# Optimization experiments

Measured on AMD Instinct MI355X. Metric: run time of the kernel, lower is better.

## Reference

```python
import jax, jax.numpy as jnp
import numpy as np

L, B, P, D, H, DH, KV, M, S, A = 12, 8, 800, 1024, 8, 256, 1, 4096, 50, 32
ROPE_BASE = 10000.0
NEG = -1e30


def _rms(x, w):
    return (x * jax.lax.rsqrt(jnp.mean(x * x, -1, keepdims=True) + 1e-6)) * (1.0 + w)


def _rope(x, cos, sin):
    # x: [B,h,S,DH]; cos/sin: [B,1,S,DH//2]
    x1, x2 = jnp.split(x, 2, axis=-1)
    return jnp.concatenate([x1 * cos - x2 * sin, x2 * cos + x1 * sin], -1)


def setup_inputs() -> dict:
    key = jax.random.key(0)
    ks = iter(jax.random.split(key, 40))
    def nrm(shape, s=0.02):
        return jax.random.normal(next(ks), shape, jnp.float32) * s
    return {
        'prefix_pad_masks': jnp.ones((B, P), jnp.bool_),
        'x_t': jax.random.normal(next(ks), (B, S, A), jnp.float32),
        'timestep': jax.random.uniform(next(ks), (B,), jnp.float32),
        'dt': jnp.full((1,), 0.1, jnp.float32),
        'cache_k': nrm((L, B, KV, P, DH), 1.0),
        'cache_v': nrm((L, B, KV, P, DH), 1.0),
        'w_act_in': nrm((A, D)), 'b_act_in': jnp.zeros((D,), jnp.float32),
        'w_t1': nrm((D, D)), 'b_t1': jnp.zeros((D,), jnp.float32),
        'w_t2': nrm((D, D)), 'b_t2': jnp.zeros((D,), jnp.float32),
        'ln1_w': jnp.zeros((L, D), jnp.float32),
        'ada1_w': nrm((L, D, D)),
        'ln2_w': jnp.zeros((L, D), jnp.float32),
        'wq': nrm((L, D, H * DH)), 'wk': nrm((L, D, KV * DH)),
        'wv': nrm((L, D, KV * DH)), 'wo': nrm((L, H * DH, D)),
        'wg': nrm((L, D, M)), 'wu': nrm((L, D, M)), 'wd': nrm((L, M, D)),
        'lnf_w': jnp.zeros((D,), jnp.float32), 'adaf_w': nrm((D, D)),
        'w_act_out': nrm((D, A)), 'b_act_out': jnp.zeros((A,), jnp.float32),
    }


def reference(prefix_pad_masks, x_t, timestep, dt, cache_k, cache_v,
              w_act_in, b_act_in, w_t1, b_t1, w_t2, b_t2,
              ln1_w, ada1_w, ln2_w, wq, wk, wv, wo, wg, wu, wd,
              lnf_w, adaf_w, w_act_out, b_act_out):
    b, s, _ = x_t.shape
    p = prefix_pad_masks.shape[1]
    # --- embed_suffix: action projection + sinusoidal time -> MLP -> adaRMS cond ---
    suffix = x_t @ w_act_in + b_act_in                              # [B,S,D]
    half = D // 2
    freqs = jnp.exp(-jnp.log(jnp.float32(10000.0)) * jnp.arange(half, dtype=jnp.float32) / half)
    ang = timestep[:, None] * freqs[None, :]
    temb = jnp.concatenate([jnp.sin(ang), jnp.cos(ang)], -1)        # [B,D]
    cond = jax.nn.silu(temb @ w_t1 + b_t1) @ w_t2 + b_t2            # adarms_cond [B,D]
    # --- prefix-suffix 2D attention mask (make_att_2d_masks_trt) ---
    suffix_pad = jnp.ones((b, s), jnp.int32)
    suffix_att = jnp.concatenate([jnp.ones((b, 1), jnp.int32), jnp.zeros((b, s - 1), jnp.int32)], 1)
    cums = jnp.cumsum(suffix_att, 1)
    att2d = cums[:, None, :] <= cums[:, :, None]
    pad2d = (suffix_pad[:, None, :] * suffix_pad[:, :, None]).astype(bool)
    pre2d = jnp.broadcast_to(prefix_pad_masks[:, None, :], (b, s, p))
    full = jnp.concatenate([pre2d, att2d & pad2d], 2)               # [B,S,P+S]
    bias = jnp.where(full, 0.0, NEG)[:, None, :, :].astype(jnp.float32)
    # --- position ids: prefix offset + suffix cumsum - 1 ---
    offs = jnp.sum(prefix_pad_masks.astype(jnp.int32), -1)[:, None]
    pos = offs + jnp.cumsum(suffix_pad, 1) - 1                      # [B,S]
    inv = 1.0 / (ROPE_BASE ** (jnp.arange(0, DH, 2, dtype=jnp.float32) / DH))
    rang = pos[..., None].astype(jnp.float32) * inv                 # [B,S,DH/2]
    cos = jnp.cos(rang)[:, None]
    sin = jnp.sin(rang)[:, None]
    # --- gemma expert (eager attention over KV cache + suffix) ---
    h = suffix * jnp.sqrt(jnp.float32(D))
    def layer(hc, xs):
        l1, a1, l2, Wq, Wk, Wv, Wo, Wg, Wu, Wd, ck, cv = xs
        x = _rms(hc, l1) * (1.0 + (cond @ a1)[:, None, :])
        q = (x @ Wq).reshape(b, s, H, DH).transpose(0, 2, 1, 3)
        k = (x @ Wk).reshape(b, s, KV, DH).transpose(0, 2, 1, 3)
        v = (x @ Wv).reshape(b, s, KV, DH).transpose(0, 2, 1, 3)
        q = _rope(q, cos, sin)
        k = _rope(k, cos, sin)
        kf = jnp.repeat(jnp.concatenate([ck, k], 2), H // KV, 1)    # [B,H,P+S,DH]
        vf = jnp.repeat(jnp.concatenate([cv, v], 2), H // KV, 1)
        sc = jnp.einsum('bhsd,bhtd->bhst', q, kf) / jnp.sqrt(jnp.float32(DH)) + bias
        at = jax.nn.softmax(sc, -1)
        o = jnp.einsum('bhst,bhtd->bhsd', at, vf).transpose(0, 2, 1, 3).reshape(b, s, H * DH)
        hc = hc + o @ Wo
        x2 = _rms(hc, l2)
        hc = hc + (jax.nn.gelu(x2 @ Wg, approximate=True) * (x2 @ Wu)) @ Wd
        return hc, None
    h, _ = jax.lax.scan(layer, h, (ln1_w, ada1_w, ln2_w, wq, wk, wv, wo, wg, wu, wd, cache_k, cache_v))
    hf = _rms(h, lnf_w) * (1.0 + (cond @ adaf_w)[:, None, :])
    v_t = hf[:, -S:].astype(jnp.float32) @ w_act_out + b_act_out    # action_out_proj
    return x_t + dt.reshape(1, 1, 1) * v_t                          # Euler step
```

## Files before the change

kernel.cpp:

```cpp
#include <hip/hip_runtime.h>
#include <hip/hip_bf16.h>
#include <math.h>

#define NLAYER 12
#define NB 8
#define NP 800
#define ND 1024
#define NH 8
#define NDH 256
#define NM 4096
#define NS 50
#define NA 32
#define NKEYS 850
#define KPAD 896
#define NCH 7

typedef unsigned short ushort_t;
typedef unsigned int u32;
using f32x4  = __attribute__((ext_vector_type(4))) float;
using short8 = __attribute__((ext_vector_type(8))) short;

__device__ __forceinline__ u32 pack_bf2(float lo, float hi) {
  u32 a = __float_as_uint(lo);
  u32 b = __float_as_uint(hi);
  a += 0x7fffu + ((a >> 16) & 1u);
  b += 0x7fffu + ((b >> 16) & 1u);
  return (a >> 16) | (b & 0xffff0000u);
}
__device__ __forceinline__ ushort_t bf1(float x) {
  u32 a = __float_as_uint(x);
  a += 0x7fffu + ((a >> 16) & 1u);
  return (ushort_t)(a >> 16);
}
__device__ __forceinline__ float ubf(ushort_t h) {
  return __uint_as_float(((u32)h) << 16);
}
__device__ __forceinline__ void async_cp16(const void* g, const void* l) {
  __builtin_amdgcn_global_load_lds(
      (const __attribute__((address_space(1))) u32*)g,
      (__attribute__((address_space(3))) u32*)l, 16, 0, 0);
}
#define SWZ(row, c) ((c) ^ (((row) & 7) << 3))


__global__ void cvt_permute_kernel(const float* __restrict__ src, ushort_t* __restrict__ dst, long nrows) {
  long idx = (long)blockIdx.x * 256 + threadIdx.x;
  long row = idx >> 5;
  int t = (int)(idx & 31);
  if (row >= nrows) return;
  const float* s = src + row * 256 + t * 4;
  float4 lo = *reinterpret_cast<const float4*>(s);
  float4 hi = *reinterpret_cast<const float4*>(s + 128);
  ushort_t* d = dst + row * 256 + t * 8;
  *reinterpret_cast<uint4*>(d) =
      make_uint4(pack_bf2(lo.x, hi.x), pack_bf2(lo.y, hi.y),
                 pack_bf2(lo.z, hi.z), pack_bf2(lo.w, hi.w));
}

template<int MODE>
__global__ __launch_bounds__(256) void transpose_cvt(
    const float* __restrict__ src, long sz, ushort_t* __restrict__ dst, long dz,
    int R, int C, int ldd, int halfOff) {
  __shared__ float Ls[64][65];
  const float* s = src + (long)blockIdx.z * sz;
  ushort_t* d    = dst + (long)blockIdx.z * dz;
  int c0 = blockIdx.x * 64, r0 = blockIdx.y * 64;
  int t = threadIdx.x;
  int rr = t >> 4;
  int cc = (t & 15) * 4;
#pragma unroll
  for (int j = 0; j < 4; ++j) {
    int rl = rr + j * 16;
    int r = r0 + rl;
    float4 v = make_float4(0.f, 0.f, 0.f, 0.f);
    if (r < R) v = *reinterpret_cast<const float4*>(s + (long)r * C + c0 + cc);
    Ls[rl][cc] = v.x; Ls[rl][cc+1] = v.y; Ls[rl][cc+2] = v.z; Ls[rl][cc+3] = v.w;
  }
  __syncthreads();
  int dr = t >> 2;
  int rc = (t & 3) * 16;
  int cg = c0 + dr;
  long orow;
  if (MODE == 0)      orow = cg;
  else if (MODE == 1) orow = ((long)(cg >> 5) << 6) + (cg & 31) + halfOff;
  else                orow = (long)(cg & ~255) + ((cg & 127) << 1) + ((cg >> 7) & 1);
  ushort_t* drow = d + orow * ldd + r0 + rc;
#pragma unroll
  for (int i = 0; i < 16; i += 2) {
    int sr = r0 + rc + i;
    if (sr < R) {
      u32 p = pack_bf2(Ls[rc + i][dr], Ls[rc + i + 1][dr]);
      *reinterpret_cast<u32*>(drow + i) = p;
    }
  }
}


__global__ void temb_kernel(const float* __restrict__ ts, float* __restrict__ temb) {
  int idx = blockIdx.x * 256 + threadIdx.x;
  if (idx >= NB * ND) return;
  int b = idx >> 10, d = idx & 1023;
  int i = d & 511;
  float f = __expf(-logf(10000.f) * (float)i / 512.f);
  float ang = ts[b] * f;
  temb[idx] = (d < 512) ? sinf(ang) : cosf(ang);
}

__global__ void suffix_kernel(const float* __restrict__ x_t, const float* __restrict__ w,
                              const float* __restrict__ bias, float* __restrict__ h) {
  int m = blockIdx.x;
  __shared__ float xs[NA];
  if (threadIdx.x < NA) xs[threadIdx.x] = x_t[m * NA + threadIdx.x];
  __syncthreads();
  for (int n = threadIdx.x; n < ND; n += 256) {
    float acc = bias[n];
#pragma unroll
    for (int k = 0; k < NA; ++k) acc += xs[k] * w[k * ND + n];
    h[m * ND + n] = acc * 32.0f;
  }
}

__global__ void rope_table_kernel(float* __restrict__ cosT, float* __restrict__ sinT) {
  int idx = blockIdx.x * 256 + threadIdx.x;
  if (idx >= NS * 128) return;
  int s = idx >> 7, i = idx & 127;
  float inv = __expf(-(float)(2 * i) / 256.f * logf(10000.f));
  float ang = (float)(NP + s) * inv;
  cosT[idx] = cosf(ang);
  sinT[idx] = sinf(ang);
}

template<bool BFOUT>
__global__ void rms_kernel(float* __restrict__ hin, const float* __restrict__ slabs,
                           const float* __restrict__ w,
                           const float* __restrict__ ada, void* __restrict__ outv) {
  int m = blockIdx.x;
  int b = m / NS;
  int d0 = threadIdx.x * 4;
  float4 v = *reinterpret_cast<const float4*>(hin + (long)m * ND + d0);
  if (slabs) {
#pragma unroll
    for (int c = 0; c < 8; ++c) {
      float4 sv = *reinterpret_cast<const float4*>(slabs + ((long)c * 400 + m) * ND + d0);
      v.x += sv.x; v.y += sv.y; v.z += sv.z; v.w += sv.w;
    }
    *reinterpret_cast<float4*>(hin + (long)m * ND + d0) = v;
  }
  float ss = v.x*v.x + v.y*v.y + v.z*v.z + v.w*v.w;
#pragma unroll
  for (int off = 32; off > 0; off >>= 1) ss += __shfl_down(ss, off);
  __shared__ float red[4];
  int lane = threadIdx.x & 63, wid = threadIdx.x >> 6;
  if (lane == 0) red[wid] = ss;
  __syncthreads();
  float tot = red[0] + red[1] + red[2] + red[3];
  float r = rsqrtf(tot * (1.f / ND) + 1e-6f);
  float4 wv = *reinterpret_cast<const float4*>(w + d0);
  float4 o;
  o.x = v.x * r * (1.f + wv.x);
  o.y = v.y * r * (1.f + wv.y);
  o.z = v.z * r * (1.f + wv.z);
  o.w = v.w * r * (1.f + wv.w);
  if (ada) {
    float4 av = *reinterpret_cast<const float4*>(ada + (long)b * ND + d0);
    o.x *= (1.f + av.x); o.y *= (1.f + av.y); o.z *= (1.f + av.z); o.w *= (1.f + av.w);
  }
  if (BFOUT) {
    *reinterpret_cast<uint2*>((ushort_t*)outv + (long)m * ND + d0) =
        make_uint2(pack_bf2(o.x, o.y), pack_bf2(o.z, o.w));
  } else {
    *reinterpret_cast<float4*>((float*)outv + (long)m * ND + d0) = o;
  }
}

__global__ void final_fused(const float* __restrict__ hin, const float* __restrict__ slabs,
                            const float* __restrict__ lnf,
                            const float* __restrict__ adaf, const float* __restrict__ w,
                            const float* __restrict__ bias, const float* __restrict__ x_t,
                            const float* __restrict__ dt, float* __restrict__ out) {
  int m = blockIdx.x;
  int b = m / NS;
  int d0 = threadIdx.x * 4;
  __shared__ float hfs[ND];
  __shared__ float red[256];
  float4 v = *reinterpret_cast<const float4*>(hin + (long)m * ND + d0);
#pragma unroll
  for (int c = 0; c < 8; ++c) {
    float4 sv = *reinterpret_cast<const float4*>(slabs + ((long)c * 400 + m) * ND + d0);
    v.x += sv.x; v.y += sv.y; v.z += sv.z; v.w += sv.w;
  }
  float ss = v.x*v.x + v.y*v.y + v.z*v.z + v.w*v.w;
#pragma unroll
  for (int off = 32; off > 0; off >>= 1) ss += __shfl_down(ss, off);
  __shared__ float red4[4];
  int lane = threadIdx.x & 63, wid = threadIdx.x >> 6;
  if (lane == 0) red4[wid] = ss;
  __syncthreads();
  float tot = red4[0] + red4[1] + red4[2] + red4[3];
  float r = rsqrtf(tot * (1.f / ND) + 1e-6f);
  float4 wv = *reinterpret_cast<const float4*>(lnf + d0);
  float4 av = *reinterpret_cast<const float4*>(adaf + (long)b * ND + d0);
  hfs[d0]     = v.x * r * (1.f + wv.x) * (1.f + av.x);
  hfs[d0 + 1] = v.y * r * (1.f + wv.y) * (1.f + av.y);
  hfs[d0 + 2] = v.z * r * (1.f + wv.z) * (1.f + av.z);
  hfs[d0 + 3] = v.w * r * (1.f + wv.w) * (1.f + av.w);
  __syncthreads();
  int a = threadIdx.x & 31;
  int kg = threadIdx.x >> 5;
  float acc = 0.f;
  for (int k = kg; k < ND; k += 8) acc += hfs[k] * w[k * NA + a];
  red[threadIdx.x] = acc;
  __syncthreads();
// ... 131 lines not shown
  const int ci1 = 256 + ci0;
  const int row1 = ci1 >> 3;
  const int kc1 = (((ci1 & 7) ^ (row1 & 7)) << 3);
  int gra0 = m0 + row0; if (gra0 > M - 1) gra0 = M - 1;
  int gra1 = m0 + row1; if (gra1 > M - 1) gra1 = M - 1;
  const int n_0 = n0 + row0;
  const int n_1 = n0 + row1;

  auto stage = [&](int buf, int k0) {
    async_cp16(A + (long)gra0 * lda + k0 + kc0, (const char*)As[buf] + ci0 * 16);
    async_cp16(B + (long)n_0 * ldb + k0 + kc0, (const char*)Bs[buf] + ci0 * 16);
    async_cp16(A + (long)gra1 * lda + k0 + kc1, (const char*)As[buf] + ci1 * 16);
    async_cp16(B + (long)n_1 * ldb + k0 + kc1, (const char*)Bs[buf] + ci1 * 16);
  };

  stage(0, 0);
  __syncthreads();
  int cur = 0;
  for (int t = 0; t < 16; ++t) {
    if (t + 1 < 16) stage(cur ^ 1, (t + 1) * 64);
    const ushort_t* Ac = As[cur];
    const ushort_t* Bc = Bs[cur];
#pragma unroll
    for (int ks = 0; ks < 2; ++ks) {
      short8 af[2], bf[2];
#pragma unroll
      for (int mi = 0; mi < 2; ++mi) {
        int row = wm + mi * 16 + l15;
        af[mi] = *reinterpret_cast<const short8*>(&Ac[row * 64 + SWZ(row, ks * 32 + l4 * 8)]);
      }
#pragma unroll
      for (int ni = 0; ni < 2; ++ni) {
        int row = wn + ni * 16 + l15;
        bf[ni] = *reinterpret_cast<const short8*>(&Bc[row * 64 + SWZ(row, ks * 32 + l4 * 8)]);
      }
#pragma unroll
      for (int mi = 0; mi < 2; ++mi)
#pragma unroll
        for (int ni = 0; ni < 2; ++ni)
          acc[mi][ni] = __builtin_amdgcn_mfma_f32_16x16x32_bf16(af[mi], bf[ni], acc[mi][ni], 0, 0, 0);
    }
    __syncthreads();
    cur ^= 1;
  }

#pragma unroll
  for (int mi = 0; mi < 2; ++mi) {
#pragma unroll
    for (int ni = 0; ni < 2; ++ni) {
      int col = n0 + wn + ni * 16 + l15;
      int rb  = m0 + wm + mi * 16 + l4 * 4;
      float pv[4];
#pragma unroll
      for (int r = 0; r < 4; ++r) pv[r] = __shfl_xor(acc[mi][ni][r], 1);
#pragma unroll
      for (int r = 0; r < 4; ++r) {
        int row = rb + r;
        if (row >= 400) continue;
        int b = row / NS, s = row - b * NS;
        float v = acc[mi][ni][r];
        if (col < 2304) {
          int j = col & 255;
          int i = j >> 1;
          float c = cosT[s * 128 + i], sn = sinT[s * 128 + i];
          float o = (col & 1) ? (v * c + pv[r] * sn) : (v * c - pv[r] * sn);
          if (col < 2048)
            qTo[((long)((b << 3) + (col >> 8)) * NS + s) * 256 + j] = bf1(o);
          else
            k_new[(long)row * 256 + j] = bf1(o);
        } else {
          vT_l[((long)(b * 256 + (col - 2304))) * KPAD + NP + s] = bf1(v);
        }
      }
    }
  }
}

__global__ __launch_bounds__(256) void flash3_kernel(
    const ushort_t* __restrict__ qT,
    const ushort_t* __restrict__ kcache_l,
    const ushort_t* __restrict__ k_new,
    const ushort_t* __restrict__ vT_l,
    const ushort_t* __restrict__ zpad,
    ushort_t* __restrict__ opart, float* __restrict__ mpart, float* __restrict__ lpart) {
  const int flat = blockIdx.x + 64 * blockIdx.y;
  const int wgid = (flat & 7) * 56 + (flat >> 3);
  const int bh = wgid & 63;
  const int ch = wgid >> 6;
  const int b  = bh >> 3;
  const int tid = threadIdx.x;
  const int lane = tid & 63;
  const int w = tid >> 6;
  const int wm = (w >> 1) * 32;
  const int wnK = (w & 1) * 64;
  const int wnV = (w & 1) * 64;
  const int l15 = lane & 15;
  const int l4  = lane >> 4;

  __shared__ __align__(16) char lds[51200];
  ushort_t* KV0 = (ushort_t*)lds;
  ushort_t* KV1 = (ushort_t*)(lds + 16384);
  ushort_t* Ps  = (ushort_t*)(lds + 32768);
  float* SMm = (float*)(lds + 50176);
  float* SMl = (float*)(lds + 50688);

  short8 qf[4][2][2];
  {
    const ushort_t* qbase = qT + (long)bh * NS * 256;
#pragma unroll
    for (int mi = 0; mi < 2; ++mi) {
      int row = wm + mi * 16 + l15;
      int qr = row < NS ? row : NS - 1;
      const ushort_t* qrow = qbase + (long)qr * 256;
#pragma unroll
      for (int s = 0; s < 4; ++s)
#pragma unroll
        for (int ks = 0; ks < 2; ++ks)
          qf[s][mi][ks] = *reinterpret_cast<const short8*>(qrow + s * 64 + ks * 32 + l4 * 8);
    }
  }

  auto stageK = [&](ushort_t* buf, int s) {
#pragma unroll
    for (int i = 0; i < 4; ++i) {
      int ci = i * 256 + tid;
      int key = ch * 128 + (ci >> 3);
      int seg = (ci ^ (ci >> 3)) & 7;
      const ushort_t* src;
      if (key < NP)         src = kcache_l + ((long)(b * NP + key)) * 256 + s * 64 + seg * 8;
      else if (key < NKEYS) src = k_new + ((long)(b * NS + key - NP)) * 256 + s * 64 + seg * 8;
      else                  src = zpad + seg * 8;
      async_cp16(src, (char*)buf + ci * 16);
    }
  };
  auto stageV = [&](ushort_t* buf, int p) {
    int dh = p >> 1, ks2 = p & 1;
#pragma unroll
    for (int i = 0; i < 4; ++i) {
      int ci = i * 256 + tid;
      int dout = dh * 128 + (ci >> 3);
      int seg = (ci ^ (ci >> 3)) & 7;
      async_cp16(vT_l + ((long)(b * 256 + dout)) * KPAD + ch * 128 + ks2 * 64 + seg * 8,
                 (char*)buf + ci * 16);
    }
  };

  f32x4 s2[2][4] = {};
  stageK(KV0, 0);
  __syncthreads();
#pragma unroll
  for (int s = 0; s < 4; ++s) {
    ushort_t* buf = (s & 1) ? KV1 : KV0;
    ushort_t* nxt = (s & 1) ? KV0 : KV1;
    if (s < 3) stageK(nxt, s + 1);
    __builtin_amdgcn_s_setprio(1);
#pragma unroll
    for (int ks = 0; ks < 2; ++ks) {
      short8 bf[4];
#pragma unroll
      for (int ni = 0; ni < 4; ++ni) {
        int row = wnK + ni * 16 + l15;
        bf[ni] = *reinterpret_cast<const short8*>(&buf[row * 64 + SWZ(row, ks * 32 + l4 * 8)]);
      }
#pragma unroll
      for (int mi = 0; mi < 2; ++mi)
#pragma unroll
        for (int ni = 0; ni < 4; ++ni)
// ... 51 lines not shown
#pragma unroll
  for (int mi = 0; mi < 2; ++mi)
#pragma unroll
    for (int ni = 0; ni < 4; ++ni) {
      int colp = wnK + ni * 16 + l15;
#pragma unroll
      for (int r = 0; r < 4; ++r) {
        float e = __expf(s2[mi][ni][r] - mrow[mi][r]);
        Ps[(wm + mi * 16 + l4 * 4 + r) * 136 + colp] = bf1(e);
        sum[mi][r] += e;
      }
    }
#pragma unroll
  for (int off = 1; off < 16; off <<= 1)
#pragma unroll
    for (int mi = 0; mi < 2; ++mi)
#pragma unroll
      for (int r = 0; r < 4; ++r)
        sum[mi][r] += __shfl_xor(sum[mi][r], off);
  if (l15 == 0) {
#pragma unroll
    for (int mi = 0; mi < 2; ++mi)
#pragma unroll
      for (int r = 0; r < 4; ++r)
        SMl[(w & 1) * 64 + wm + mi * 16 + l4 * 4 + r] = sum[mi][r];
  }
  __syncthreads();
  if ((w & 1) == 0 && l15 == 0) {
#pragma unroll
    for (int mi = 0; mi < 2; ++mi)
#pragma unroll
      for (int r = 0; r < 4; ++r) {
        int row = wm + mi * 16 + l4 * 4 + r;
        if (row < NS) {
          mpart[((long)bh * NCH + ch) * NS + row] = mrow[mi][r];
          lpart[((long)bh * NCH + ch) * NS + row] = SMl[row] + SMl[64 + row];
        }
      }
  }

  f32x4 o2[2][2][4] = {};
#pragma unroll
  for (int p = 0; p < 4; ++p) {
    ushort_t* buf = (p & 1) ? KV1 : KV0;
    ushort_t* nxt = (p & 1) ? KV0 : KV1;
    if (p < 3) stageV(nxt, p + 1);
    int dh = p >> 1, ks2 = p & 1;
    __builtin_amdgcn_s_setprio(1);
#pragma unroll
    for (int ks = 0; ks < 2; ++ks) {
      short8 af[2], bf[4];
#pragma unroll
      for (int mi = 0; mi < 2; ++mi)
        af[mi] = *reinterpret_cast<const short8*>(&Ps[(wm + mi * 16 + l15) * 136 + ks2 * 64 + ks * 32 + l4 * 8]);
#pragma unroll
      for (int ni = 0; ni < 4; ++ni) {
        int row = wnV + ni * 16 + l15;
        bf[ni] = *reinterpret_cast<const short8*>(&buf[row * 64 + SWZ(row, ks * 32 + l4 * 8)]);
      }
#pragma unroll
      for (int mi = 0; mi < 2; ++mi)
#pragma unroll
        for (int ni = 0; ni < 4; ++ni)
          o2[mi][dh][ni] = __builtin_amdgcn_mfma_f32_16x16x32_bf16(af[mi], bf[ni], o2[mi][dh][ni], 0, 0, 0);
    }
    __builtin_amdgcn_s_setprio(0);
    __syncthreads();
  }

#pragma unroll
  for (int mi = 0; mi < 2; ++mi)
#pragma unroll
    for (int dh = 0; dh < 2; ++dh)
#pragma unroll
      for (int ni = 0; ni < 4; ++ni) {
        int col = dh * 128 + wnV + ni * 16 + l15;
#pragma unroll
        for (int r = 0; r < 4; ++r) {
          int row = wm + mi * 16 + l4 * 4 + r;
          if (row < NS)
            opart[(((long)bh * NCH + ch) * NS + row) * 256 + col] = bf1(o2[mi][dh][ni][r]);
        }
      }
}

__global__ void att_combine(const ushort_t* __restrict__ opart, const float* __restrict__ mpart,
                            const float* __restrict__ lpart, ushort_t* __restrict__ o_buf) {
  int blk = blockIdx.x;
  int b = blk / NS, s = blk - b * NS;
  int d = threadIdx.x;
  for (int h = 0; h < NH; ++h) {
    int bh = b * NH + h;
    float mv[NCH];
    float m = -1e30f;
#pragma unroll
    for (int c = 0; c < NCH; ++c) {
      mv[c] = mpart[((long)bh * NCH + c) * NS + s];
      m = fmaxf(m, mv[c]);
    }
    float den = 0.f, o = 0.f;
#pragma unroll
    for (int c = 0; c < NCH; ++c) {
      float wgt = __expf(mv[c] - m);
      den += wgt * lpart[((long)bh * NCH + c) * NS + s];
      o   += wgt * ubf(opart[(((long)bh * NCH + c) * NS + s) * 256 + d]);
    }
    o_buf[(long)blk * 2048 + h * 256 + d] = bf1(o / den);
  }
}

__global__ __launch_bounds__(256) void gemm64G(
    const ushort_t* __restrict__ A, const ushort_t* __restrict__ B,
    ushort_t* __restrict__ C, int M, int K, int lda, int ldb, int ldc) {
  const int flat = blockIdx.x + 7 * blockIdx.y;
  const int wgid = (flat & 7) * 112 + (flat >> 3);
  const int m0 = (wgid % 7) * 64;
  const int n0 = (wgid / 7) * 64;
  const int tid = threadIdx.x;
  const int lane = tid & 63;
  const int wbase = tid & 192;
  const int wid = wbase >> 6;
  const int l15 = lane & 15;
  const int l4  = lane >> 4;

  __shared__ ushort_t As[2][64 * 64];
  __shared__ ushort_t Bs[2][64 * 64];

  f32x4 acc[4] = {};

  const int ci0 = wbase + lane;
  const int row0 = ci0 >> 3;
  const int kc0 = (((ci0 & 7) ^ (row0 & 7)) << 3);
  const int ci1 = 256 + ci0;
  const int row1 = ci1 >> 3;
  const int kc1 = (((ci1 & 7) ^ (row1 & 7)) << 3);
  int gra0 = m0 + row0; if (gra0 > M - 1) gra0 = M - 1;
  int gra1 = m0 + row1; if (gra1 > M - 1) gra1 = M - 1;

  auto stage = [&](int buf, int k0) {
    async_cp16(A + (long)gra0 * lda + k0 + kc0, (const char*)As[buf] + ci0 * 16);
    async_cp16(B + (long)(n0 + row0) * ldb + k0 + kc0, (const char*)Bs[buf] + ci0 * 16);
    async_cp16(A + (long)gra1 * lda + k0 + kc1, (const char*)As[buf] + ci1 * 16);
    async_cp16(B + (long)(n0 + row1) * ldb + k0 + kc1, (const char*)Bs[buf] + ci1 * 16);
  };

  const int nt = K >> 6;
  stage(0, 0);
  __syncthreads();
  int cur = 0;
  for (int t = 0; t < nt; ++t) {
    if (t + 1 < nt) stage(cur ^ 1, (t + 1) * 64);
    const ushort_t* Ac = As[cur];
    const ushort_t* Bc = Bs[cur];
#pragma unroll
    for (int ks = 0; ks < 2; ++ks) {
      int arow = wid * 16 + l15;
      short8 af = *reinterpret_cast<const short8*>(&Ac[arow * 64 + SWZ(arow, ks * 32 + l4 * 8)]);
#pragma unroll
      for (int ni = 0; ni < 4; ++ni) {
        int row = ni * 16 + l15;
        short8 bf = *reinterpret_cast<const short8*>(&Bc[row * 64 + SWZ(row, ks * 32 + l4 * 8)]);
        acc[ni] = __builtin_amdgcn_mfma_f32_16x16x32_bf16(af, bf, acc[ni], 0, 0, 0);
      }
    }
    __syncthreads();
    cur ^= 1;
  }

#pragma unroll
  for (int ni = 0; ni < 2; ++ni) {
    int col = (n0 >> 1) + ni * 16 + l15;
    int rb  = m0 + wid * 16 + l4 * 4;
#pragma unroll
    for (int r = 0; r < 4; ++r) {
      int row = rb + r;
      if (row >= M) continue;
      float g = acc[ni][r];
      float u = acc[ni + 2][r];
      float inner = 0.7978845608028654f * (g + 0.044715f * g * g * g);
      float t = g / (1.f + __expf(-2.f * inner));
      C[(long)row * ldc + col] = bf1(t * u);
    }
  }
}

template<int EPI>
__global__ __launch_bounds__(256)
void gemm_f32_kernel(const float* __restrict__ A,
                     const float* __restrict__ B1,
                     float* __restrict__ C,
// ... 154 lines not shown
      for (int ni = 0; ni < 2; ++ni)
        bfr[ni] = *reinterpret_cast<const short8*>(&Bs[wn + ni*16 + l15][ks*32 + l4*8]);
#pragma unroll
      for (int mi = 0; mi < 2; ++mi)
#pragma unroll
        for (int ni = 0; ni < 2; ++ni)
          acc[mi][ni] = __builtin_amdgcn_mfma_f32_16x16x32_bf16(af[mi], bfr[ni], acc[mi][ni], 0, 0, 0);
    }
    __syncthreads();
  }

#pragma unroll
  for (int mi = 0; mi < 2; ++mi) {
#pragma unroll
    for (int ni = 0; ni < 2; ++ni) {
      int col = n0 + wn + ni * 16 + l15;
      int rb  = m0 + wm + mi * 16 + l4 * 4;
#pragma unroll
      for (int r = 0; r < 4; ++r) {
        int row = rb + r;
        if (row < M && col < N)
          atomicAdd(&Cb[(long)row * ldc + col], acc[mi][ni][r]);
      }
    }
  }
}

extern "C" void kernel_launch(void* const* d_in, const int* in_sizes, int n_in,
                              void* d_out, int out_size, void* d_ws, size_t ws_size,
                              hipStream_t stream) {
  (void)in_sizes; (void)n_in; (void)out_size; (void)ws_size;
  const float* x_t      = (const float*)d_in[1];
  const float* tstep    = (const float*)d_in[2];
  const float* dtp      = (const float*)d_in[3];
  const float* cache_k  = (const float*)d_in[4];
  const float* cache_v  = (const float*)d_in[5];
  const float* w_act_in = (const float*)d_in[6];
  const float* b_act_in = (const float*)d_in[7];
  const float* w_t1     = (const float*)d_in[8];
  const float* b_t1     = (const float*)d_in[9];
  const float* w_t2     = (const float*)d_in[10];
  const float* b_t2     = (const float*)d_in[11];
  const float* ln1_w    = (const float*)d_in[12];
  const float* ada1_w   = (const float*)d_in[13];
  const float* ln2_w    = (const float*)d_in[14];
  const float* wq       = (const float*)d_in[15];
  const float* wk       = (const float*)d_in[16];
  const float* wv       = (const float*)d_in[17];
  const float* wo       = (const float*)d_in[18];
  const float* wg       = (const float*)d_in[19];
  const float* wu       = (const float*)d_in[20];
  const float* wd       = (const float*)d_in[21];
  const float* lnf_w    = (const float*)d_in[22];
  const float* adaf_w   = (const float*)d_in[23];
  const float* wao      = (const float*)d_in[24];
  const float* bao      = (const float*)d_in[25];
  float* outp = (float*)d_out;

  char* p = (char*)d_ws;
  auto alloc = [&](size_t bytes) { char* r = p; p += (bytes + 255) & ~(size_t)255; return r; };

  ushort_t* wqkvT  = (ushort_t*)alloc((size_t)12 * 2560 * 1024 * 2);
  ushort_t* woT    = (ushort_t*)alloc((size_t)12 * 1024 * 2048 * 2);
  ushort_t* wguT   = (ushort_t*)alloc((size_t)12 * 8192 * 1024 * 2);
  ushort_t* wdT    = (ushort_t*)alloc((size_t)12 * 1024 * 4096 * 2);
  ushort_t* kcache = (ushort_t*)alloc((size_t)12 * 8 * NP * 256 * 2);
  ushort_t* vT     = (ushort_t*)alloc((size_t)12 * 8 * 256 * KPAD * 2);
  ushort_t* qT     = (ushort_t*)alloc((size_t)64 * NS * 256 * 2);
  ushort_t* k_new  = (ushort_t*)alloc((size_t)400 * 256 * 2);
  ushort_t* opart  = (ushort_t*)alloc((size_t)64 * NCH * NS * 256 * 2);
  float*    mpart  = (float*)alloc((size_t)64 * NCH * NS * 4);
  float*    lpart  = (float*)alloc((size_t)64 * NCH * NS * 4);
  float*    woP    = (float*)alloc((size_t)8 * 400 * 1024 * 4);
  float*    wdP    = (float*)alloc((size_t)8 * 400 * 1024 * 4);
  ushort_t* o_buf  = (ushort_t*)alloc((size_t)400 * 2048 * 2);
  ushort_t* t_buf  = (ushort_t*)alloc((size_t)400 * 4096 * 2);
  ushort_t* x_buf  = (ushort_t*)alloc((size_t)400 * 1024 * 2);
  float*    h_buf  = (float*)alloc((size_t)400 * 1024 * 4);
  float*    temb   = (float*)alloc(8 * 1024 * 4);
  float*    tmp    = (float*)alloc(8 * 1024 * 4);
  float*    cond   = (float*)alloc(8 * 1024 * 4);
  float*    ada_all= (float*)alloc((size_t)12 * 8 * 1024 * 4);
  float*    adaf_o = (float*)alloc(8 * 1024 * 4);
  float*    cosT   = (float*)alloc(NS * 128 * 4);
  float*    sinT   = (float*)alloc(NS * 128 * 4);
  ushort_t* zpad   = (ushort_t*)alloc(512 * 2);

  hipMemsetAsync(zpad, 0, 512 * 2, stream);
  hipMemsetAsync(ada_all, 0, ((size_t)12 * 8 * 1024 + 8 * 1024) * 4, stream);

  cvt_permute_kernel<<<9600, 256, 0, stream>>>(cache_k, kcache, (long)12 * 8 * NP);
  transpose_cvt<2><<<dim3(32, 16, 12), 256, 0, stream>>>(wq, (long)1024 * 2048, wqkvT, (long)2560 * 1024, 1024, 2048, 1024, 0);
  transpose_cvt<2><<<dim3(4, 16, 12), 256, 0, stream>>>(wk, (long)1024 * 256, wqkvT + (long)2048 * 1024, (long)2560 * 1024, 1024, 256, 1024, 0);
  transpose_cvt<0><<<dim3(4, 16, 12), 256, 0, stream>>>(wv, (long)1024 * 256, wqkvT + (long)2304 * 1024, (long)2560 * 1024, 1024, 256, 1024, 0);
  transpose_cvt<0><<<dim3(16, 32, 12), 256, 0, stream>>>(wo, (long)2048 * 1024, woT, (long)1024 * 2048, 2048, 1024, 2048, 0);
  transpose_cvt<1><<<dim3(64, 16, 12), 256, 0, stream>>>(wg, (long)1024 * 4096, wguT, (long)8192 * 1024, 1024, 4096, 1024, 0);
  transpose_cvt<1><<<dim3(64, 16, 12), 256, 0, stream>>>(wu, (long)1024 * 4096, wguT, (long)8192 * 1024, 1024, 4096, 1024, 32);
  transpose_cvt<0><<<dim3(16, 64, 12), 256, 0, stream>>>(wd, (long)4096 * 1024, wdT, (long)1024 * 4096, 4096, 1024, 4096, 0);
  transpose_cvt<0><<<dim3(4, 13, 96), 256, 0, stream>>>(cache_v, (long)NP * 256, vT, (long)256 * KPAD, NP, 256, KPAD, 0);

  temb_kernel<<<32, 256, 0, stream>>>(tstep, temb);
  suffix_kernel<<<400, 256, 0, stream>>>(x_t, w_act_in, b_act_in, h_buf);
  rope_table_kernel<<<25, 256, 0, stream>>>(cosT, sinT);
  gemm_f32_kernel<2><<<dim3(1, 16, 1), 256, 0, stream>>>(temb, w_t1, tmp, NB, ND, ND, ND, ND, ND, b_t1);
  gemm_f32_kernel<1><<<dim3(1, 16, 1), 256, 0, stream>>>(tmp, w_t2, cond, NB, ND, ND, ND, ND, ND, b_t2);
  gemm_f32sk<<<dim3(1, 16, 48), 256, 0, stream>>>(cond, ada1_w, (long)ND * ND, ada_all, (long)NB * ND, NB, ND, ND, ND, ND, ND, 4);
  gemm_f32sk<<<dim3(1, 16, 4), 256, 0, stream>>>(cond, adaf_w, 0, adaf_o, 0, NB, ND, ND, ND, ND, ND, 4);

  for (int l = 0; l < NLAYER; ++l) {
    ushort_t* vT_l = vT + (long)l * 8 * 256 * KPAD;
    rms_kernel<true><<<400, 256, 0, stream>>>(
        h_buf, l == 0 ? nullptr : wdP, ln1_w + (long)l * ND, ada_all + (long)l * NB * ND, x_buf);
    gemm64rope<<<dim3(7, 40, 1), 256, 0, stream>>>(
        x_buf, wqkvT + (long)l * 2560 * 1024, cosT, sinT, qT, k_new, vT_l);
    flash3_kernel<<<dim3(64, NCH, 1), 256, 0, stream>>>(
        qT, kcache + (long)l * 8 * NP * 256, k_new, vT_l, zpad, opart, mpart, lpart);
    att_combine<<<400, 256, 0, stream>>>(opart, mpart, lpart, o_buf);
    gemm64slab<<<dim3(7, 16, 8), 256, 0, stream>>>(
        o_buf, woT + (long)l * 1024 * 2048, woP, 400, 1024, 2048, 2048, 2048, 1024, 256);
    rms_kernel<true><<<400, 256, 0, stream>>>(
        h_buf, woP, ln2_w + (long)l * ND, nullptr, x_buf);
    gemm64G<<<dim3(7, 128, 1), 256, 0, stream>>>(
        x_buf, wguT + (long)l * 8192 * 1024, t_buf, 400, 1024, 1024, 1024, 4096);
    gemm64slab<<<dim3(7, 16, 8), 256, 0, stream>>>(
        t_buf, wdT + (long)l * 1024 * 4096, wdP, 400, 1024, 4096, 4096, 4096, 1024, 512);
  }

  final_fused<<<400, 256, 0, stream>>>(h_buf, wdP, lnf_w, adaf_o, wao, bao, x_t, dtp, outp);
}
```

Baseline: 1.769 ms.

## Fuse prep conversions into one launch and merge attention combine into flash kernel

Merges the per-weight conversion/transpose kernels into a single dispatcher kernel and the temb, rope table and suffix kernels into one prep kernel. Removes the separate att_combine launch by having the last-finishing flash block per batch-head (tracked with an atomic counter) combine the partial outputs. This cuts launch count and per-layer kernel boundaries, but the in-kernel combine runs on only one block per head and serially over rows, which may create tail work.

```diff
diff --git a/kernel.cpp b/kernel.cpp
--- a/kernel.cpp
+++ b/kernel.cpp
@@ -43,28 +43,13 @@
 #define SWZ(row, c) ((c) ^ (((row) & 7) << 3))
 
 
-__global__ void cvt_permute_kernel(const float* __restrict__ src, ushort_t* __restrict__ dst, long nrows) {
-  long idx = (long)blockIdx.x * 256 + threadIdx.x;
-  long row = idx >> 5;
-  int t = (int)(idx & 31);
-  if (row >= nrows) return;
-  const float* s = src + row * 256 + t * 4;
-  float4 lo = *reinterpret_cast<const float4*>(s);
-  float4 hi = *reinterpret_cast<const float4*>(s + 128);
-  ushort_t* d = dst + row * 256 + t * 8;
-  *reinterpret_cast<uint4*>(d) =
-      make_uint4(pack_bf2(lo.x, hi.x), pack_bf2(lo.y, hi.y),
-                 pack_bf2(lo.z, hi.z), pack_bf2(lo.w, hi.w));
-}
-
-template<int MODE>
-__global__ __launch_bounds__(256) void transpose_cvt(
-    const float* __restrict__ src, long sz, ushort_t* __restrict__ dst, long dz,
-    int R, int C, int ldd, int halfOff) {
-  __shared__ float Ls[64][65];
-  const float* s = src + (long)blockIdx.z * sz;
-  ushort_t* d    = dst + (long)blockIdx.z * dz;
-  int c0 = blockIdx.x * 64, r0 = blockIdx.y * 64;
+__device__ __forceinline__ void transpose_body(
+    const float* __restrict__ src, ushort_t* __restrict__ dst,
+    int R, int C, int ldd, int mode, int halfOff,
+    int bx, int by, int bz, long sz, long dz, float* Ls) {
+  const float* s = src + (long)bz * sz;
+  ushort_t* d    = dst + (long)bz * dz;
+  int c0 = bx * 64, r0 = by * 64;
   int t = threadIdx.x;
   int rr = t >> 4;
   int cc = (t & 15) * 4;
@@ -74,60 +59,145 @@
     int r = r0 + rl;
     float4 v = make_float4(0.f, 0.f, 0.f, 0.f);
     if (r < R) v = *reinterpret_cast<const float4*>(s + (long)r * C + c0 + cc);
-    Ls[rl][cc] = v.x; Ls[rl][cc+1] = v.y; Ls[rl][cc+2] = v.z; Ls[rl][cc+3] = v.w;
+    Ls[rl * 65 + cc] = v.x; Ls[rl * 65 + cc + 1] = v.y;
+    Ls[rl * 65 + cc + 2] = v.z; Ls[rl * 65 + cc + 3] = v.w;
   }
   __syncthreads();
   int dr = t >> 2;
   int rc = (t & 3) * 16;
   int cg = c0 + dr;
   long orow;
-  if (MODE == 0)      orow = cg;
-  else if (MODE == 1) orow = ((long)(cg >> 5) << 6) + (cg & 31) + halfOff;
+  if (mode == 0)      orow = cg;
+  else if (mode == 1) orow = ((long)(cg >> 5) << 6) + (cg & 31) + halfOff;
   else                orow = (long)(cg & ~255) + ((cg & 127) << 1) + ((cg >> 7) & 1);
   ushort_t* drow = d + orow * ldd + r0 + rc;
 #pragma unroll
   for (int i = 0; i < 16; i += 2) {
     int sr = r0 + rc + i;
     if (sr < R) {
-      u32 p = pack_bf2(Ls[rc + i][dr], Ls[rc + i + 1][dr]);
-      *reinterpret_cast<u32*>(drow + i) = p;
-    }
-  }
-}
-
-
-__global__ void temb_kernel(const float* __restrict__ ts, float* __restrict__ temb) {
-  int idx = blockIdx.x * 256 + threadIdx.x;
-  if (idx >= NB * ND) return;
-  int b = idx >> 10, d = idx & 1023;
-  int i = d & 511;
-  float f = __expf(-logf(10000.f) * (float)i / 512.f);
-  float ang = ts[b] * f;
-  temb[idx] = (d < 512) ? sinf(ang) : cosf(ang);
-}
-
-__global__ void suffix_kernel(const float* __restrict__ x_t, const float* __restrict__ w,
-                              const float* __restrict__ bias, float* __restrict__ h) {
-  int m = blockIdx.x;
+      u32 pk = pack_bf2(Ls[(rc + i) * 65 + dr], Ls[(rc + i + 1) * 65 + dr]);
+      *reinterpret_cast<u32*>(drow + i) = pk;
+    }
+  }
+}
+
+__global__ __launch_bounds__(256) void conv_all(
+    const float* __restrict__ cache_k, ushort_t* __restrict__ kcache,
+    const float* __restrict__ wq, const float* __restrict__ wk,
+    const float* __restrict__ wv, const float* __restrict__ wo,
+    const float* __restrict__ wg, const float* __restrict__ wu,
+    const float* __restrict__ wd, const float* __restrict__ cache_v,
+    ushort_t* __restrict__ wqkvT, ushort_t* __restrict__ woT,
+    ushort_t* __restrict__ wguT, ushort_t* __restrict__ wdT,
+    ushort_t* __restrict__ vT) {
+  __shared__ float Ls[64 * 65];
+  int f = blockIdx.x;
+  if (f < 9600) {
+    long idx = (long)f * 256 + threadIdx.x;
+    long row = idx >> 5;
+    int t = (int)(idx & 31);
+    if (row >= (long)12 * 8 * NP) return;
+    const float* s = cache_k + row * 256 + t * 4;
+    float4 lo = *reinterpret_cast<const float4*>(s);
+    float4 hi = *reinterpret_cast<const float4*>(s + 128);
+    ushort_t* d = kcache + row * 256 + t * 8;
+    *reinterpret_cast<uint4*>(d) =
+        make_uint4(pack_bf2(lo.x, hi.x), pack_bf2(lo.y, hi.y),
+                   pack_bf2(lo.z, hi.z), pack_bf2(lo.w, hi.w));
+    return;
+  }
+  f -= 9600;
+  if (f < 6144) {
+    int z = f >> 9, r = f & 511;
+    transpose_body(wq, wqkvT, 1024, 2048, 1024, 2, 0, r & 31, r >> 5, z,
+                   (long)1024 * 2048, (long)2560 * 1024, Ls);
+    return;
+  }
+  f -= 6144;
+  if (f < 768) {
+    int z = f >> 6, r = f & 63;
+    transpose_body(wk, wqkvT + (long)2048 * 1024, 1024, 256, 1024, 2, 0, r & 3, r >> 2, z,
+                   (long)1024 * 256, (long)2560 * 1024, Ls);
+    return;
+  }
+  f -= 768;
+  if (f < 768) {
+    int z = f >> 6, r = f & 63;
+    transpose_body(wv, wqkvT + (long)2304 * 1024, 1024, 256, 1024, 0, 0, r & 3, r >> 2, z,
+                   (long)1024 * 256, (long)2560 * 1024, Ls);
+    return;
+  }
+  f -= 768;
+  if (f < 6144) {
+    int z = f >> 9, r = f & 511;
+    transpose_body(wo, woT, 2048, 1024, 2048, 0, 0, r & 15, r >> 4, z,
+                   (long)2048 * 1024, (long)1024 * 2048, Ls);
+    return;
+  }
+  f -= 6144;
+  if (f < 12288) {
+    int z = f >> 10, r = f & 1023;
+    transpose_body(wg, wguT, 1024, 4096, 1024, 1, 0, r & 63, r >> 6, z,
+                   (long)1024 * 4096, (long)8192 * 1024, Ls);
+    return;
+  }
+  f -= 12288;
+  if (f < 12288) {
+    int z = f >> 10, r = f & 1023;
+    transpose_body(wu, wguT, 1024, 4096, 1024, 1, 32, r & 63, r >> 6, z,
+                   (long)1024 * 4096, (long)8192 * 1024, Ls);
+    return;
+  }
+  f -= 12288;
+  if (f < 12288) {
+    int z = f >> 10, r = f & 1023;
+    transpose_body(wd, wdT, 4096, 1024, 4096, 0, 0, r & 15, r >> 4, z,
+                   (long)4096 * 1024, (long)1024 * 4096, Ls);
+    return;
+  }
+  f -= 12288;
+  {
+    int z = f / 52, r = f % 52;
+    transpose_body(cache_v, vT, NP, 256, KPAD, 0, 0, r & 3, r >> 2, z,
+                   (long)NP * 256, (long)256 * KPAD, Ls);
+  }
+}
+
+__global__ void prep_kernel(const float* __restrict__ ts, float* __restrict__ temb,
+                            float* __restrict__ cosT, float* __restrict__ sinT,
+                            const float* __restrict__ x_t, const float* __restrict__ w_act,
+                            const float* __restrict__ b_act, float* __restrict__ h) {
+  int blk = blockIdx.x;
+  if (blk < 32) {
+    int idx = blk * 256 + threadIdx.x;
+    if (idx >= NB * ND) return;
+    int b = idx >> 10, d = idx & 1023;
+    int i = d & 511;
+    float fr = __expf(-logf(10000.f) * (float)i / 512.f);
+    float ang = ts[b] * fr;
+    temb[idx] = (d < 512) ? sinf(ang) : cosf(ang);
+    return;
+  }
+  if (blk < 57) {
+    int idx = (blk - 32) * 256 + threadIdx.x;
+    if (idx >= NS * 128) return;
+    int s = idx >> 7, i = idx & 127;
+    float inv = __expf(-(float)(2 * i) / 256.f * logf(10000.f));
+    float ang = (float)(NP + s) * inv;
+    cosT[idx] = cosf(ang);
+    sinT[idx] = sinf(ang);
+    return;
+  }
+  int m = blk - 57;
   __shared__ float xs[NA];
   if (threadIdx.x < NA) xs[threadIdx.x] = x_t[m * NA + threadIdx.x];
   __syncthreads();
   for (int n = threadIdx.x; n < ND; n += 256) {
-    float acc = bias[n];
-#pragma unroll
-    for (int k = 0; k < NA; ++k) acc += xs[k] * w[k * ND + n];
+    float acc = b_act[n];
+#pragma unroll
+    for (int k = 0; k < NA; ++k) acc += xs[k] * w_act[k * ND + n];
     h[m * ND + n] = acc * 32.0f;
   }
-}
-
-__global__ void rope_table_kernel(float* __restrict__ cosT, float* __restrict__ sinT) {
-  int idx = blockIdx.x * 256 + threadIdx.x;
-  if (idx >= NS * 128) return;
-  int s = idx >> 7, i = idx & 127;
-  float inv = __expf(-(float)(2 * i) / 256.f * logf(10000.f));
-  float ang = (float)(NP + s) * inv;
-  cosT[idx] = cosf(ang);
-  sinT[idx] = sinf(ang);
 }
 
 template<bool BFOUT>
@@ -425,7 +495,8 @@
     const ushort_t* __restrict__ k_new,
     const ushort_t* __restrict__ vT_l,
     const ushort_t* __restrict__ zpad,
-    ushort_t* __restrict__ opart, float* __restrict__ mpart, float* __restrict__ lpart) {
+    ushort_t* __restrict__ opart, float* __restrict__ mpart, float* __restrict__ lpart,
+    u32* __restrict__ cnt, ushort_t* __restrict__ o_buf) {
   const int flat = blockIdx.x + 64 * blockIdx.y;
   const int wgid = (flat & 7) * 56 + (flat >> 3);
   const int bh = wgid & 63;
@@ -643,15 +714,21 @@
             opart[(((long)bh * NCH + ch) * NS + row) * 256 + col] = bf1(o2[mi][dh][ni][r]);
         }
       }
-}
-
-__global__ void att_combine(const ushort_t* __restrict__ opart, const float* __restrict__ mpart,
-                            const float* __restrict__ lpart, ushort_t* __restrict__ o_buf) {
-  int blk = blockIdx.x;
-  int b = blk / NS, s = blk - b * NS;
-  int d = threadIdx.x;
-  for (int h = 0; h < NH; ++h) {
-    int bh = b * NH + h;
+
+  __syncthreads();
+  volatile u32* flag = (volatile u32*)lds;
+  if (tid == 0) {
+    __threadfence();
+    u32 old = atomicAdd(&cnt[bh], 1u);
+    *flag = (old == NCH - 1) ? 1u : 0u;
+  }
+  __syncthreads();
+  if (*flag == 0u) return;
+  __threadfence();
+
+  float* wf = (float*)(lds + 256);
+  if (tid < NS) {
+    int s = tid;
     float mv[NCH];
     float m = -1e30f;
 #pragma unroll
@@ -659,14 +736,26 @@
       mv[c] = mpart[((long)bh * NCH + c) * NS + s];
       m = fmaxf(m, mv[c]);
     }
-    float den = 0.f, o = 0.f;
+    float den = 0.f, wloc[NCH];
 #pragma unroll
     for (int c = 0; c < NCH; ++c) {
       float wgt = __expf(mv[c] - m);
+      wloc[c] = wgt;
       den += wgt * lpart[((long)bh * NCH + c) * NS + s];
-      o   += wgt * ubf(opart[(((long)bh * NCH + c) * NS + s) * 256 + d]);
-    }
-    o_buf[(long)blk * 2048 + h * 256 + d] = bf1(o / den);
+    }
+    float inv = 1.f / den;
+#pragma unroll
+    for (int c = 0; c < NCH; ++c) wf[c * 64 + s] = wloc[c] * inv;
+  }
+  __syncthreads();
+  int d = tid;
+  int hh = bh & 7;
+  for (int s = 0; s < NS; ++s) {
+    float o = 0.f;
+#pragma unroll
+    for (int c = 0; c < NCH; ++c)
+      o += wf[c * 64 + s] * ubf(opart[(((long)bh * NCH + c) * NS + s) * 256 + d]);
+    o_buf[((long)(b * NS + s)) * 2048 + hh * 256 + d] = bf1(o);
   }
 }
 
@@ -987,26 +1076,19 @@
   float*    cond   = (float*)alloc(8 * 1024 * 4);
   float*    ada_all= (float*)alloc((size_t)12 * 8 * 1024 * 4);
   float*    adaf_o = (float*)alloc(8 * 1024 * 4);
+  u32*      cnt    = (u32*)alloc((size_t)12 * 64 * 4);
   float*    cosT   = (float*)alloc(NS * 128 * 4);
   float*    sinT   = (float*)alloc(NS * 128 * 4);
   ushort_t* zpad   = (ushort_t*)alloc(512 * 2);
 
   hipMemsetAsync(zpad, 0, 512 * 2, stream);
-  hipMemsetAsync(ada_all, 0, ((size_t)12 * 8 * 1024 + 8 * 1024) * 4, stream);
-
-  cvt_permute_kernel<<<9600, 256, 0, stream>>>(cache_k, kcache, (long)12 * 8 * NP);
-  transpose_cvt<2><<<dim3(32, 16, 12), 256, 0, stream>>>(wq, (long)1024 * 2048, wqkvT, (long)2560 * 1024, 1024, 2048, 1024, 0);
-  transpose_cvt<2><<<dim3(4, 16, 12), 256, 0, stream>>>(wk, (long)1024 * 256, wqkvT + (long)2048 * 1024, (long)2560 * 1024, 1024, 256, 1024, 0);
-  transpose_cvt<0><<<dim3(4, 16, 12), 256, 0, stream>>>(wv, (long)1024 * 256, wqkvT + (long)2304 * 1024, (long)2560 * 1024, 1024, 256, 1024, 0);
-  transpose_cvt<0><<<dim3(16, 32, 12), 256, 0, stream>>>(wo, (long)2048 * 1024, woT, (long)1024 * 2048, 2048, 1024, 2048, 0);
-  transpose_cvt<1><<<dim3(64, 16, 12), 256, 0, stream>>>(wg, (long)1024 * 4096, wguT, (long)8192 * 1024, 1024, 4096, 1024, 0);
-  transpose_cvt<1><<<dim3(64, 16, 12), 256, 0, stream>>>(wu, (long)1024 * 4096, wguT, (long)8192 * 1024, 1024, 4096, 1024, 32);
-  transpose_cvt<0><<<dim3(16, 64, 12), 256, 0, stream>>>(wd, (long)4096 * 1024, wdT, (long)1024 * 4096, 4096, 1024, 4096, 0);
-  transpose_cvt<0><<<dim3(4, 13, 96), 256, 0, stream>>>(cache_v, (long)NP * 256, vT, (long)256 * KPAD, NP, 256, KPAD, 0);
-
-  temb_kernel<<<32, 256, 0, stream>>>(tstep, temb);
-  suffix_kernel<<<400, 256, 0, stream>>>(x_t, w_act_in, b_act_in, h_buf);
-  rope_table_kernel<<<25, 256, 0, stream>>>(cosT, sinT);
+  hipMemsetAsync(ada_all, 0,
+                 ((size_t)12 * 8 * 1024 + 8 * 1024) * 4 + (size_t)12 * 64 * 4, stream);
+
+  conv_all<<<65280, 256, 0, stream>>>(cache_k, kcache, wq, wk, wv, wo, wg, wu, wd, cache_v,
+                                      wqkvT, woT, wguT, wdT, vT);
+
+  prep_kernel<<<457, 256, 0, stream>>>(tstep, temb, cosT, sinT, x_t, w_act_in, b_act_in, h_buf);
   gemm_f32_kernel<2><<<dim3(1, 16, 1), 256, 0, stream>>>(temb, w_t1, tmp, NB, ND, ND, ND, ND, ND, b_t1);
   gemm_f32_kernel<1><<<dim3(1, 16, 1), 256, 0, stream>>>(tmp, w_t2, cond, NB, ND, ND, ND, ND, ND, b_t2);
   gemm_f32sk<<<dim3(1, 16, 48), 256, 0, stream>>>(cond, ada1_w, (long)ND * ND, ada_all, (long)NB * ND, NB, ND, ND, ND, ND, ND, 4);
@@ -1019,8 +1101,8 @@
     gemm64rope<<<dim3(7, 40, 1), 256, 0, stream>>>(
         x_buf, wqkvT + (long)l * 2560 * 1024, cosT, sinT, qT, k_new, vT_l);
     flash3_kernel<<<dim3(64, NCH, 1), 256, 0, stream>>>(
-        qT, kcache + (long)l * 8 * NP * 256, k_new, vT_l, zpad, opart, mpart, lpart);
-    att_combine<<<400, 256, 0, stream>>>(opart, mpart, lpart, o_buf);
+        qT, kcache + (long)l * 8 * NP * 256, k_new, vT_l, zpad,
+        opart, mpart, lpart, cnt + l * 64, o_buf);
     gemm64slab<<<dim3(7, 16, 8), 256, 0, stream>>>(
         o_buf, woT + (long)l * 1024 * 2048, woP, 400, 1024, 2048, 2048, 2048, 1024, 256);
     rms_kernel<true><<<400, 256, 0, stream>>>(
```

Measured after the change: 1.907 ms. +7.8%, slower.

## Fuse split-K attention combine into flash kernel via last-block counter; merge prep kernels

Applied to the files above, without the earlier changes.

Removes the separate att_combine launch per layer. Each flash3 workgroup atomically increments a per-(b,h) counter, and the last chunk to finish merges all partial outputs into o_buf using LDS-staged weights. The three small setup kernels (temb, rope table, suffix projection) are also merged into one launch. This saves launch overhead and a dependent kernel per layer, at the cost of a serial tail in the last block per head, which reads 7 partials over a 50-row loop.

```diff
diff --git a/kernel.cpp b/kernel.cpp
--- a/kernel.cpp
+++ b/kernel.cpp
@@ -95,39 +95,41 @@
   }
 }
 
-
-__global__ void temb_kernel(const float* __restrict__ ts, float* __restrict__ temb) {
-  int idx = blockIdx.x * 256 + threadIdx.x;
-  if (idx >= NB * ND) return;
-  int b = idx >> 10, d = idx & 1023;
-  int i = d & 511;
-  float f = __expf(-logf(10000.f) * (float)i / 512.f);
-  float ang = ts[b] * f;
-  temb[idx] = (d < 512) ? sinf(ang) : cosf(ang);
-}
-
-__global__ void suffix_kernel(const float* __restrict__ x_t, const float* __restrict__ w,
-                              const float* __restrict__ bias, float* __restrict__ h) {
-  int m = blockIdx.x;
+__global__ void prep_kernel(const float* __restrict__ ts, float* __restrict__ temb,
+                            float* __restrict__ cosT, float* __restrict__ sinT,
+                            const float* __restrict__ x_t, const float* __restrict__ w_act,
+                            const float* __restrict__ b_act, float* __restrict__ h) {
+  int blk = blockIdx.x;
+  if (blk < 32) {
+    int idx = blk * 256 + threadIdx.x;
+    if (idx >= NB * ND) return;
+    int b = idx >> 10, d = idx & 1023;
+    int i = d & 511;
+    float fr = __expf(-logf(10000.f) * (float)i / 512.f);
+    float ang = ts[b] * fr;
+    temb[idx] = (d < 512) ? sinf(ang) : cosf(ang);
+    return;
+  }
+  if (blk < 57) {
+    int idx = (blk - 32) * 256 + threadIdx.x;
+    if (idx >= NS * 128) return;
+    int s = idx >> 7, i = idx & 127;
+    float inv = __expf(-(float)(2 * i) / 256.f * logf(10000.f));
+    float ang = (float)(NP + s) * inv;
+    cosT[idx] = cosf(ang);
+    sinT[idx] = sinf(ang);
+    return;
+  }
+  int m = blk - 57;
   __shared__ float xs[NA];
   if (threadIdx.x < NA) xs[threadIdx.x] = x_t[m * NA + threadIdx.x];
   __syncthreads();
   for (int n = threadIdx.x; n < ND; n += 256) {
-    float acc = bias[n];
-#pragma unroll
-    for (int k = 0; k < NA; ++k) acc += xs[k] * w[k * ND + n];
+    float acc = b_act[n];
+#pragma unroll
+    for (int k = 0; k < NA; ++k) acc += xs[k] * w_act[k * ND + n];
     h[m * ND + n] = acc * 32.0f;
   }
-}
-
-__global__ void rope_table_kernel(float* __restrict__ cosT, float* __restrict__ sinT) {
-  int idx = blockIdx.x * 256 + threadIdx.x;
-  if (idx >= NS * 128) return;
-  int s = idx >> 7, i = idx & 127;
-  float inv = __expf(-(float)(2 * i) / 256.f * logf(10000.f));
-  float ang = (float)(NP + s) * inv;
-  cosT[idx] = cosf(ang);
-  sinT[idx] = sinf(ang);
 }
 
 template<bool BFOUT>
@@ -425,7 +427,8 @@
     const ushort_t* __restrict__ k_new,
     const ushort_t* __restrict__ vT_l,
     const ushort_t* __restrict__ zpad,
-    ushort_t* __restrict__ opart, float* __restrict__ mpart, float* __restrict__ lpart) {
+    ushort_t* __restrict__ opart, float* __restrict__ mpart, float* __restrict__ lpart,
+    u32* __restrict__ cnt, ushort_t* __restrict__ o_buf) {
   const int flat = blockIdx.x + 64 * blockIdx.y;
   const int wgid = (flat & 7) * 56 + (flat >> 3);
   const int bh = wgid & 63;
@@ -643,15 +646,21 @@
             opart[(((long)bh * NCH + ch) * NS + row) * 256 + col] = bf1(o2[mi][dh][ni][r]);
         }
       }
-}
-
-__global__ void att_combine(const ushort_t* __restrict__ opart, const float* __restrict__ mpart,
-                            const float* __restrict__ lpart, ushort_t* __restrict__ o_buf) {
-  int blk = blockIdx.x;
-  int b = blk / NS, s = blk - b * NS;
-  int d = threadIdx.x;
-  for (int h = 0; h < NH; ++h) {
-    int bh = b * NH + h;
+
+  __syncthreads();
+  volatile u32* flag = (volatile u32*)lds;
+  if (tid == 0) {
+    __threadfence();
+    u32 old = atomicAdd(&cnt[bh], 1u);
+    *flag = (old == NCH - 1) ? 1u : 0u;
+  }
+  __syncthreads();
+  if (*flag == 0u) return;
+  __threadfence();
+
+  float* wf = (float*)(lds + 256);
+  if (tid < NS) {
+    int s = tid;
     float mv[NCH];
     float m = -1e30f;
 #pragma unroll
@@ -659,14 +668,26 @@
       mv[c] = mpart[((long)bh * NCH + c) * NS + s];
       m = fmaxf(m, mv[c]);
     }
-    float den = 0.f, o = 0.f;
+    float den = 0.f, wloc[NCH];
 #pragma unroll
     for (int c = 0; c < NCH; ++c) {
       float wgt = __expf(mv[c] - m);
+      wloc[c] = wgt;
       den += wgt * lpart[((long)bh * NCH + c) * NS + s];
-      o   += wgt * ubf(opart[(((long)bh * NCH + c) * NS + s) * 256 + d]);
-    }
-    o_buf[(long)blk * 2048 + h * 256 + d] = bf1(o / den);
+    }
+    float inv = 1.f / den;
+#pragma unroll
+    for (int c = 0; c < NCH; ++c) wf[c * 64 + s] = wloc[c] * inv;
+  }
+  __syncthreads();
+  int d = tid;
+  int hh = bh & 7;
+  for (int s = 0; s < NS; ++s) {
+    float o = 0.f;
+#pragma unroll
+    for (int c = 0; c < NCH; ++c)
+      o += wf[c * 64 + s] * ubf(opart[(((long)bh * NCH + c) * NS + s) * 256 + d]);
+    o_buf[((long)(b * NS + s)) * 2048 + hh * 256 + d] = bf1(o);
   }
 }
 
@@ -987,12 +1008,14 @@
   float*    cond   = (float*)alloc(8 * 1024 * 4);
   float*    ada_all= (float*)alloc((size_t)12 * 8 * 1024 * 4);
   float*    adaf_o = (float*)alloc(8 * 1024 * 4);
+  u32*      cnt    = (u32*)alloc((size_t)12 * 64 * 4);
   float*    cosT   = (float*)alloc(NS * 128 * 4);
   float*    sinT   = (float*)alloc(NS * 128 * 4);
   ushort_t* zpad   = (ushort_t*)alloc(512 * 2);
 
   hipMemsetAsync(zpad, 0, 512 * 2, stream);
-  hipMemsetAsync(ada_all, 0, ((size_t)12 * 8 * 1024 + 8 * 1024) * 4, stream);
+  hipMemsetAsync(ada_all, 0,
+                 ((size_t)12 * 8 * 1024 + 8 * 1024) * 4 + (size_t)12 * 64 * 4, stream);
 
   cvt_permute_kernel<<<9600, 256, 0, stream>>>(cache_k, kcache, (long)12 * 8 * NP);
   transpose_cvt<2><<<dim3(32, 16, 12), 256, 0, stream>>>(wq, (long)1024 * 2048, wqkvT, (long)2560 * 1024, 1024, 2048, 1024, 0);
@@ -1004,9 +1027,7 @@
   transpose_cvt<0><<<dim3(16, 64, 12), 256, 0, stream>>>(wd, (long)4096 * 1024, wdT, (long)1024 * 4096, 4096, 1024, 4096, 0);
   transpose_cvt<0><<<dim3(4, 13, 96), 256, 0, stream>>>(cache_v, (long)NP * 256, vT, (long)256 * KPAD, NP, 256, KPAD, 0);
 
-  temb_kernel<<<32, 256, 0, stream>>>(tstep, temb);
-  suffix_kernel<<<400, 256, 0, stream>>>(x_t, w_act_in, b_act_in, h_buf);
-  rope_table_kernel<<<25, 256, 0, stream>>>(cosT, sinT);
+  prep_kernel<<<457, 256, 0, stream>>>(tstep, temb, cosT, sinT, x_t, w_act_in, b_act_in, h_buf);
   gemm_f32_kernel<2><<<dim3(1, 16, 1), 256, 0, stream>>>(temb, w_t1, tmp, NB, ND, ND, ND, ND, ND, b_t1);
   gemm_f32_kernel<1><<<dim3(1, 16, 1), 256, 0, stream>>>(tmp, w_t2, cond, NB, ND, ND, ND, ND, ND, b_t2);
   gemm_f32sk<<<dim3(1, 16, 48), 256, 0, stream>>>(cond, ada1_w, (long)ND * ND, ada_all, (long)NB * ND, NB, ND, ND, ND, ND, ND, 4);
@@ -1019,8 +1040,8 @@
     gemm64rope<<<dim3(7, 40, 1), 256, 0, stream>>>(
         x_buf, wqkvT + (long)l * 2560 * 1024, cosT, sinT, qT, k_new, vT_l);
     flash3_kernel<<<dim3(64, NCH, 1), 256, 0, stream>>>(
-        qT, kcache + (long)l * 8 * NP * 256, k_new, vT_l, zpad, opart, mpart, lpart);
-    att_combine<<<400, 256, 0, stream>>>(opart, mpart, lpart, o_buf);
+        qT, kcache + (long)l * 8 * NP * 256, k_new, vT_l, zpad,
+        opart, mpart, lpart, cnt + l * 64, o_buf);
     gemm64slab<<<dim3(7, 16, 8), 256, 0, stream>>>(
         o_buf, woT + (long)l * 1024 * 2048, woP, 400, 1024, 2048, 2048, 2048, 1024, 256);
     rms_kernel<true><<<400, 256, 0, stream>>>(
```

New measurement: 2.095 ms. 1.18x slower.
